# Performance work log

Hardware: AMD Instinct MI355X
Metric: run time of the kernel (lower is better)

The kernel has to match this reference:

```python
import jax, jax.numpy as jnp
import numpy as np

B, C, H, W = 8, 64, 256, 256


def setup_inputs() -> dict:
    key = jax.random.key(0)
    k1, k2, k3 = jax.random.split(key, 3)
    phi = jax.random.normal(k1, (B, 2, H, W), dtype=jnp.float32) * 2.0
    x_enc = jax.random.normal(k2, (B, C, H, W), dtype=jnp.float32)
    m = jax.random.uniform(k3, (B, 1, H, W), dtype=jnp.float32)
    return {"phi": phi, "x_enc": x_enc, "m": m}


def _grid_sample_bilinear_zeros(x, grid):
    """torch.nn.functional.grid_sample defaults: bilinear, zeros padding,
    align_corners=False. x: [b,c,h,w], grid: [b,h,w,2] in [-1,1] (x,y order)."""
    b, c, h, w = x.shape
    # unnormalize (align_corners=False convention)
    ix = (grid[..., 0] + 1.0) * (0.5 * w) - 0.5  # [b,h,w]
    iy = (grid[..., 1] + 1.0) * (0.5 * h) - 0.5
    x0 = jnp.floor(ix)
    y0 = jnp.floor(iy)
    x1 = x0 + 1.0
    y1 = y0 + 1.0
    wx1 = ix - x0
    wx0 = 1.0 - wx1
    wy1 = iy - y0
    wy0 = 1.0 - wy1

    bidx = jnp.arange(b)[:, None, None]

    def corner(yy, xx, wgt):
        valid = (xx >= 0) & (xx < w) & (yy >= 0) & (yy < h)
        xc = jnp.clip(xx, 0, w - 1).astype(jnp.int32)
        yc = jnp.clip(yy, 0, h - 1).astype(jnp.int32)
        v = x[bidx, :, yc, xc]  # gather -> [b,h,w,c]
        return v * (wgt * valid.astype(x.dtype))[..., None]

    out = (corner(y0, x0, wy0 * wx0) + corner(y0, x1, wy0 * wx1)
           + corner(y1, x0, wy1 * wx0) + corner(y1, x1, wy1 * wx1))  # [b,h,w,c]
    return jnp.transpose(out, (0, 3, 1, 2))  # [b,c,h,w]


def reference(phi, x_enc, m):
    b, c, h, w = x_enc.shape
    # pixel coordinate grid: channel 0 = x (width), channel 1 = y (height)
    yy, xx = jnp.meshgrid(jnp.arange(h, dtype=jnp.float32),
                          jnp.arange(w, dtype=jnp.float32), indexing="ij")
    grid = jnp.stack([xx, yy], axis=0)[None]  # [1,2,h,w]
    vgrid = grid + phi                         # [b,2,h,w]
    vx = 2.0 * vgrid[:, 0] / max(w - 1, 1) - 1.0
    vy = 2.0 * vgrid[:, 1] / max(h - 1, 1) - 1.0
    vgrid = jnp.stack([vx, vy], axis=-1)       # [b,h,w,2]
    # original: phi = phi.permute(0,2,3,1); vgrid = vgrid + 2*phi
    vgrid = vgrid + 2.0 * jnp.transpose(phi, (0, 2, 3, 1))
    out = _grid_sample_bilinear_zeros(x_enc, vgrid)
    return out * m
```

## Files before the change

kernel.cpp:

```cpp
#include <hip/hip_runtime.h>
#include <hip/hip_bf16.h>

namespace {

constexpr int B = 8, C = 64, H = 256, W = 256;
constexpr int HW = H * W;

__global__ __launch_bounds__(256) void warp_kernel(
    const float* __restrict__ phi,
    const float* __restrict__ xenc,
    const float* __restrict__ mm,
    float* __restrict__ out)
{
    const int tid = blockIdx.x * 256 + threadIdx.x;
    const int w = tid & (W - 1);
    const int h = (tid >> 8) & (H - 1);
    const int b = tid >> 16;
    const int hw = h * W + w;

    const float p0 = phi[(size_t)(b * 2 + 0) * HW + hw];
    const float p1 = phi[(size_t)(b * 2 + 1) * HW + hw];
    const float mv = mm[(size_t)b * HW + hw];

    const float gx = (2.0f * ((float)w + p0)) / (float)(W - 1) - 1.0f + 2.0f * p0;
    const float gy = (2.0f * ((float)h + p1)) / (float)(H - 1) - 1.0f + 2.0f * p1;

    const float ix = (gx + 1.0f) * (0.5f * (float)W) - 0.5f;
    const float iy = (gy + 1.0f) * (0.5f * (float)H) - 0.5f;

    const float x0f = floorf(ix);
    const float y0f = floorf(iy);
    const float fx1 = ix - x0f, fx0 = 1.0f - fx1;
    const float fy1 = iy - y0f, fy0 = 1.0f - fy1;

    const float wm1 = (float)(W - 1), hm1 = (float)(H - 1);
    const int x0 = (int)fminf(fmaxf(x0f,        0.0f), wm1);
    const int x1 = (int)fminf(fmaxf(x0f + 1.0f, 0.0f), wm1);
    const int y0 = (int)fminf(fmaxf(y0f,        0.0f), hm1);
    const int y1 = (int)fminf(fmaxf(y0f + 1.0f, 0.0f), hm1);

    const bool vx0 = (x0f >= 0.0f) && (x0f < (float)W);
    const bool vx1 = (x0f + 1.0f >= 0.0f) && (x0f + 1.0f < (float)W);
    const bool vy0 = (y0f >= 0.0f) && (y0f < (float)H);
    const bool vy1 = (y0f + 1.0f >= 0.0f) && (y0f + 1.0f < (float)H);

    const float w00 = fy0 * fx0 * ((vy0 && vx0) ? mv : 0.0f);
    const float w01 = fy0 * fx1 * ((vy0 && vx1) ? mv : 0.0f);
    const float w10 = fy1 * fx0 * ((vy1 && vx0) ? mv : 0.0f);
    const float w11 = fy1 * fx1 * ((vy1 && vx1) ? mv : 0.0f);

    const bool doGather = (w00 + w01 + w10 + w11) != 0.0f;

    const int o00 = y0 * W + x0;
    const int o01 = y0 * W + x1;
    const int o10 = y1 * W + x0;
    const int o11 = y1 * W + x1;

    const float* __restrict__ xb = xenc + (size_t)b * C * HW;
    float* __restrict__ ob = out + (size_t)b * C * HW + hw;

    #pragma unroll 4
    for (int c = 0; c < C; ++c) {
        float v = 0.0f;
        if (doGather) {
            const float* __restrict__ xc = xb + (size_t)c * HW;
            v = xc[o00] * w00
              + xc[o01] * w01
              + xc[o10] * w10
              + xc[o11] * w11;
        }
        ob[(size_t)c * HW] = v;
    }
}

}

extern "C" void kernel_launch(void* const* d_in, const int* in_sizes, int n_in,
                              void* d_out, int out_size, void* d_ws, size_t ws_size,
                              hipStream_t stream) {
    const float* phi  = (const float*)d_in[0];
    const float* xenc = (const float*)d_in[1];
    const float* mm   = (const float*)d_in[2];
    float* out = (float*)d_out;

    const int pixels = B * H * W;
    warp_kernel<<<dim3(pixels / 256), dim3(256), 0, stream>>>(phi, xenc, mm, out);
}
```

Baseline: 257.5 us.

## Compact in-bounds pixels and gather across channels via shared-memory transpose tile

Each block now handles 64 pixels of one row. One wave computes the sampling weights and offsets, then compacts the in-bounds pixels into shared memory with a ballot and popcount. All four waves then gather with lanes mapped to channels, so each pixel's 64 channels are fetched in parallel. Results are transposed through a padded LDS tile and written out as coalesced float4 nontemporal stores. This targets the wasted lanes of divergent out-of-bounds threads and the scattered per-channel gathers. In exchange it adds two barriers, an LDS zero-fill, and lets only one wave of four do the coordinate math.

```diff
diff --git a/kernel.cpp b/kernel.cpp
--- a/kernel.cpp
+++ b/kernel.cpp
@@ -1,10 +1,13 @@
 #include <hip/hip_runtime.h>
-#include <hip/hip_bf16.h>
 
 namespace {
 
 constexpr int B = 8, C = 64, H = 256, W = 256;
 constexpr int HW = H * W;
+constexpr int TP = 64;
+constexpr int TSTRIDE = 68;
+
+typedef float v4f __attribute__((ext_vector_type(4)));
 
 __global__ __launch_bounds__(256) void warp_kernel(
     const float* __restrict__ phi,
@@ -12,64 +15,105 @@
     const float* __restrict__ mm,
     float* __restrict__ out)
 {
-    const int tid = blockIdx.x * 256 + threadIdx.x;
-    const int w = tid & (W - 1);
-    const int h = (tid >> 8) & (H - 1);
-    const int b = tid >> 16;
-    const int hw = h * W + w;
+    __shared__ float tile[64 * TSTRIDE];
+    __shared__ float s_w[4][TP];
+    __shared__ int   s_o[4][TP];
+    __shared__ int   s_p[TP];
+    __shared__ int   s_n;
 
-    const float p0 = phi[(size_t)(b * 2 + 0) * HW + hw];
-    const float p1 = phi[(size_t)(b * 2 + 1) * HW + hw];
-    const float mv = mm[(size_t)b * HW + hw];
+    const int t   = threadIdx.x;
+    const int bid = blockIdx.x;
+    const int wt  = bid & 3;
+    const int h   = (bid >> 2) & (H - 1);
+    const int b   = bid >> 10;
+    const int w0  = wt * 64;
 
-    const float gx = (2.0f * ((float)w + p0)) / (float)(W - 1) - 1.0f + 2.0f * p0;
-    const float gy = (2.0f * ((float)h + p1)) / (float)(H - 1) - 1.0f + 2.0f * p1;
+    {
+        v4f z = {0.f, 0.f, 0.f, 0.f};
+        for (int i = t; i < (64 * TSTRIDE) / 4; i += 256)
+            *(v4f*)&tile[i * 4] = z;
+    }
 
-    const float ix = (gx + 1.0f) * (0.5f * (float)W) - 0.5f;
-    const float iy = (gy + 1.0f) * (0.5f * (float)H) - 0.5f;
+    if (t < 64) {
+        const int lane = t;
+        const int w    = w0 + lane;
+        const int hw   = h * W + w;
 
-    const float x0f = floorf(ix);
-    const float y0f = floorf(iy);
-    const float fx1 = ix - x0f, fx0 = 1.0f - fx1;
-    const float fy1 = iy - y0f, fy0 = 1.0f - fy1;
+        const float p0 = phi[(size_t)(b * 2 + 0) * HW + hw];
+        const float p1 = phi[(size_t)(b * 2 + 1) * HW + hw];
+        const float mv = mm[(size_t)b * HW + hw];
 
-    const float wm1 = (float)(W - 1), hm1 = (float)(H - 1);
-    const int x0 = (int)fminf(fmaxf(x0f,        0.0f), wm1);
-    const int x1 = (int)fminf(fmaxf(x0f + 1.0f, 0.0f), wm1);
-    const int y0 = (int)fminf(fmaxf(y0f,        0.0f), hm1);
-    const int y1 = (int)fminf(fmaxf(y0f + 1.0f, 0.0f), hm1);
+        const float gx = (2.0f * ((float)w + p0)) / (float)(W - 1) - 1.0f + 2.0f * p0;
+        const float gy = (2.0f * ((float)h + p1)) / (float)(H - 1) - 1.0f + 2.0f * p1;
+        const float ix = (gx + 1.0f) * (0.5f * (float)W) - 0.5f;
+        const float iy = (gy + 1.0f) * (0.5f * (float)H) - 0.5f;
 
-    const bool vx0 = (x0f >= 0.0f) && (x0f < (float)W);
-    const bool vx1 = (x0f + 1.0f >= 0.0f) && (x0f + 1.0f < (float)W);
-    const bool vy0 = (y0f >= 0.0f) && (y0f < (float)H);
-    const bool vy1 = (y0f + 1.0f >= 0.0f) && (y0f + 1.0f < (float)H);
+        const float x0f = floorf(ix);
+        const float y0f = floorf(iy);
+        const float fx1 = ix - x0f, fx0 = 1.0f - fx1;
+        const float fy1 = iy - y0f, fy0 = 1.0f - fy1;
 
-    const float w00 = fy0 * fx0 * ((vy0 && vx0) ? mv : 0.0f);
-    const float w01 = fy0 * fx1 * ((vy0 && vx1) ? mv : 0.0f);
-    const float w10 = fy1 * fx0 * ((vy1 && vx0) ? mv : 0.0f);
-    const float w11 = fy1 * fx1 * ((vy1 && vx1) ? mv : 0.0f);
+        const float wm1 = (float)(W - 1), hm1 = (float)(H - 1);
+        const int x0 = (int)fminf(fmaxf(x0f,        0.0f), wm1);
+        const int x1 = (int)fminf(fmaxf(x0f + 1.0f, 0.0f), wm1);
+        const int y0 = (int)fminf(fmaxf(y0f,        0.0f), hm1);
+        const int y1 = (int)fminf(fmaxf(y0f + 1.0f, 0.0f), hm1);
 
-    const bool doGather = (w00 + w01 + w10 + w11) != 0.0f;
+        const bool vx0 = (x0f >= 0.0f) && (x0f < (float)W);
+        const bool vx1 = (x0f + 1.0f >= 0.0f) && (x0f + 1.0f < (float)W);
+        const bool vy0 = (y0f >= 0.0f) && (y0f < (float)H);
+        const bool vy1 = (y0f + 1.0f >= 0.0f) && (y0f + 1.0f < (float)H);
 
-    const int o00 = y0 * W + x0;
-    const int o01 = y0 * W + x1;
-    const int o10 = y1 * W + x0;
-    const int o11 = y1 * W + x1;
+        const float w00 = fy0 * fx0 * ((vy0 && vx0) ? mv : 0.0f);
+        const float w01 = fy0 * fx1 * ((vy0 && vx1) ? mv : 0.0f);
+        const float w10 = fy1 * fx0 * ((vy1 && vx0) ? mv : 0.0f);
+        const float w11 = fy1 * fx1 * ((vy1 && vx1) ? mv : 0.0f);
 
-    const float* __restrict__ xb = xenc + (size_t)b * C * HW;
-    float* __restrict__ ob = out + (size_t)b * C * HW + hw;
+        const bool inb = (w00 + w01 + w10 + w11) != 0.0f;
 
-    #pragma unroll 4
-    for (int c = 0; c < C; ++c) {
-        float v = 0.0f;
-        if (doGather) {
-            const float* __restrict__ xc = xb + (size_t)c * HW;
-            v = xc[o00] * w00
-              + xc[o01] * w01
-              + xc[o10] * w10
-              + xc[o11] * w11;
+        const unsigned long long mask = __ballot(inb);
+        const int pos = __popcll(mask & ((1ULL << lane) - 1ULL));
+        if (inb) {
+            s_w[0][pos] = w00;  s_w[1][pos] = w01;
+            s_w[2][pos] = w10;  s_w[3][pos] = w11;
+            s_o[0][pos] = y0 * W + x0;
+            s_o[1][pos] = y0 * W + x1;
+            s_o[2][pos] = y1 * W + x0;
+            s_o[3][pos] = y1 * W + x1;
+            s_p[pos]    = lane;
         }
-        ob[(size_t)c * HW] = v;
+        if (lane == 0) s_n = __popcll(mask);
+    }
+    __syncthreads();
+
+    {
+        const int wv   = t >> 6;
+        const int lane = t & 63;
+        const int n    = s_n;
+        const float* __restrict__ xb = xenc + ((size_t)b * C + lane) * HW;
+        for (int i = wv; i < n; i += 4) {
+            const float w00 = s_w[0][i], w01 = s_w[1][i];
+            const float w10 = s_w[2][i], w11 = s_w[3][i];
+            const int o00 = s_o[0][i], o01 = s_o[1][i];
+            const int o10 = s_o[2][i], o11 = s_o[3][i];
+            const int p   = s_p[i];
+            const float v = xb[o00] * w00 + xb[o01] * w01
+                          + xb[o10] * w10 + xb[o11] * w11;
+            tile[lane * TSTRIDE + p] = v;
+        }
+    }
+    __syncthreads();
+
+    {
+        const size_t obase = (size_t)b * C * HW + (size_t)h * W + w0;
+        const int cl = t >> 4;
+        const int p4 = (t & 15) * 4;
+        #pragma unroll
+        for (int pass = 0; pass < 4; ++pass) {
+            const int c = pass * 16 + cl;
+            v4f v = *(const v4f*)&tile[c * TSTRIDE + p4];
+            __builtin_nontemporal_store(v, (v4f*)(out + obase + (size_t)c * HW + p4));
+        }
     }
 }
 
@@ -83,6 +127,6 @@
     const float* mm   = (const float*)d_in[2];
     float* out = (float*)d_out;
 
-    const int pixels = B * H * W;
-    warp_kernel<<<dim3(pixels / 256), dim3(256), 0, stream>>>(phi, xenc, mm, out);
+    const int blocks = B * H * (W / 64);
+    warp_kernel<<<dim3(blocks), dim3(256), 0, stream>>>(phi, xenc, mm, out);
 }
```

New measurement: 244.7 us. -5.0%, faster.
